# Kernel tuning notes

Hardware: AMD Instinct MI355X
Metric: run time of the kernel (lower is better)

The kernel has to match this reference:

```python
import jax, jax.numpy as jnp
import numpy as np

N_NODES = 50000
N_EDGES = 800000
D = 128
H = 8
HD = D // H
N_NTYPES = 3
N_ETYPES = 5
LN_EPS = 1e-5


def setup_inputs() -> dict:
    key = jax.random.key(0)
    ks = jax.random.split(key, 16)
    inp = {
        "x": jax.random.normal(ks[0], (N_NODES, D), dtype=jnp.float32),
        "edge_index": jax.random.randint(ks[1], (2, N_EDGES), 0, N_NODES),
        "edge_type": jax.random.randint(ks[2], (N_EDGES,), 0, N_ETYPES),
        "node_type": jax.random.randint(ks[3], (N_NODES,), 0, N_NTYPES),
        # per-(node_type, head) QKV projections, per-(edge_type, head) K transform
        "W_Q": jax.random.normal(ks[4], (N_NTYPES, H, HD, HD), dtype=jnp.float32) * 0.02,
        "W_K": jax.random.normal(ks[5], (N_NTYPES, H, HD, HD), dtype=jnp.float32) * 0.02,
        "W_V": jax.random.normal(ks[6], (N_NTYPES, H, HD, HD), dtype=jnp.float32) * 0.02,
        "W_edge": jax.random.normal(ks[7], (N_ETYPES, H, HD, HD), dtype=jnp.float32) * 0.02,
        "mu": jnp.ones((H, N_ETYPES), dtype=jnp.float32),
        "W_out": jax.random.normal(ks[8], (D, D), dtype=jnp.float32) * 0.02,
        "b_out": jnp.zeros((D,), dtype=jnp.float32),
        "ln1_g": jnp.ones((D,), dtype=jnp.float32),
        "ln1_b": jnp.zeros((D,), dtype=jnp.float32),
        "W1": jax.random.normal(ks[9], (D, 4 * D), dtype=jnp.float32) * 0.02,
        "b1": jnp.zeros((4 * D,), dtype=jnp.float32),
        "W2": jax.random.normal(ks[10], (4 * D, D), dtype=jnp.float32) * 0.02,
        "b2": jnp.zeros((D,), dtype=jnp.float32),
        "ln2_g": jnp.ones((D,), dtype=jnp.float32),
        "ln2_b": jnp.zeros((D,), dtype=jnp.float32),
    }
    return inp


def _layer_norm(y, g, b):
    m = y.mean(-1, keepdims=True)
    v = ((y - m) ** 2).mean(-1, keepdims=True)
    return (y - m) * jax.lax.rsqrt(v + LN_EPS) * g + b


def reference(x, edge_index, edge_type, node_type,
              W_Q, W_K, W_V, W_edge, mu,
              W_out, b_out, ln1_g, ln1_b, W1, b1, W2, b2, ln2_g, ln2_b):
    N = x.shape[0]
    xh = x.reshape(N, H, HD)  # heads vectorized (concat of per-head slices)

    # type-specific QKV: small fixed loop over node types, masked select
    Q = jnp.zeros_like(xh)
    K = jnp.zeros_like(xh)
    V = jnp.zeros_like(xh)
    for t in range(N_NTYPES):
        m = (node_type == t)[:, None, None]
        Q = jnp.where(m, jnp.einsum('nhd,hdf->nhf', xh, W_Q[t]), Q)
        K = jnp.where(m, jnp.einsum('nhd,hdf->nhf', xh, W_K[t]), K)
        V = jnp.where(m, jnp.einsum('nhd,hdf->nhf', xh, W_V[t]), V)

    src, dst = edge_index[0], edge_index[1]
    q_dst = Q[dst]   # [E,H,HD]
    k_src = K[src]   # [E,H,HD]

    # edge-type-specific K transform
    kt = jnp.zeros_like(k_src)
    for et in range(N_ETYPES):
        m = (edge_type == et)[:, None, None]
        kt = jnp.where(m, jnp.einsum('ehd,hdf->ehf', k_src, W_edge[et]), kt)

    scores = (q_dst * kt).sum(-1) / jnp.sqrt(jnp.float32(HD))  # [E,H]
    scores = scores * mu[:, edge_type].T                       # mu per edge type, per head

    # sparse softmax over incoming edges of each dst node, per head
    smax = jax.ops.segment_max(scores, dst, num_segments=N)
    ex = jnp.exp(scores - smax[dst])
    den = jax.ops.segment_sum(ex, dst, num_segments=N)
    w = ex / (den[dst] + 1e-10)                                 # [E,H]

    agg = jax.ops.segment_sum(V[src] * w[..., None], dst, num_segments=N)  # [N,H,HD]
    mh = agg.reshape(N, D) @ W_out + b_out  # dropout is identity in eval

    h = _layer_norm(x + mh, ln1_g, ln1_b)
    ffn = jax.nn.gelu(h @ W1 + b1, approximate=False) @ W2 + b2
    return _layer_norm(h + ffn, ln2_g, ln2_b)
```

## Files before the change

### kernel.cpp

```cpp
#include <hip/hip_runtime.h>
#include <hip/hip_bf16.h>

#define N_NODESC 50000
#define N_EDGESC 800000
#define DD 128
#define HH 8
#define HDIM 16
#define N_NT 3
#define N_ET 5
#define NPB 196
#define NEB 400
#define NFB 512
#define WPB 912

#define KV8_OFF    ((size_t)0)
#define QT8_OFF    ((size_t)12800000)
#define XP_OFF     ((size_t)44800000)
#define AGG_OFF    ((size_t)57600000)
#define WOUTT_OFF  ((size_t)83200000)
#define W1T_OFF    ((size_t)83232768)
#define W2T_OFF    ((size_t)83363840)
#define WHPF_OFF   ((size_t)83494912)
#define EDATA_OFF  ((size_t)84183040)
#define ROWS_OFF   ((size_t)87383040)
#define ORIG_OFF   ((size_t)87583104)
#define DEG_OFF    ((size_t)87783104)
#define TOFS_OFF   ((size_t)87983104)
#define BH_OFF     ((size_t)87983168)
#define BB_OFF     ((size_t)87985536)
#define TMP_OFF    ((size_t)87988928)
#define RLOC_OFF   ((size_t)91188928)
#define CSUM_OFF   ((size_t)91389056)

using short8 = __attribute__((ext_vector_type(8))) short;
using f32x4  = __attribute__((ext_vector_type(4))) float;
using f32x2  = __attribute__((ext_vector_type(2))) float;

__device__ __forceinline__ ushort f2b(float f) {
    __hip_bfloat16 h = __float2bfloat16(f);
    return *(ushort*)&h;
}
__device__ __forceinline__ float b2f(ushort u) {
    __hip_bfloat16 h = *(__hip_bfloat16*)&u;
    return __bfloat162float(h);
}
__device__ __forceinline__ f32x2 pk0(unsigned int w) {
    return __builtin_amdgcn_cvt_pk_f32_fp8((int)w, false);
}
__device__ __forceinline__ f32x2 pk1(unsigned int w) {
    return __builtin_amdgcn_cvt_pk_f32_fp8((int)w, true);
}
__device__ __forceinline__ float gelu_f(float v) {
    const float x = v * 0.70710678118654752f;
    const float ax = fabsf(x);
    const float d = fmaf(0.3275911f, ax, 1.0f);
    float t;
    asm("v_rcp_f32 %0, %1" : "=v"(t) : "v"(d));
    float p = fmaf(1.061405429f, t, -1.453152027f);
    p = fmaf(p, t, 1.421413741f);
    p = fmaf(p, t, -0.284496736f);
    p = fmaf(p, t, 0.254829592f);
    p = p * t;
    const float e = __expf(-ax * ax);
    const float er = 1.0f - p * e;
    const float erfx = (x < 0.f) ? -er : er;
    return 0.5f * v * (1.0f + erfx);
}
__device__ __forceinline__ void ebar() {
    __builtin_amdgcn_sched_barrier(0);
    asm volatile("s_waitcnt lgkmcnt(0)" ::: "memory");
    __builtin_amdgcn_sched_barrier(0);
    __builtin_amdgcn_s_barrier();
    __builtin_amdgcn_sched_barrier(0);
}

__global__ __launch_bounds__(256) void prep_a(
    const float* __restrict__ Wout, const float* __restrict__ W1, const float* __restrict__ W2,
    const float* __restrict__ WQ, const float* __restrict__ Wk, const float* __restrict__ Wv,
    const float* __restrict__ We, const float* __restrict__ mu,
    ushort* __restrict__ Woutt, ushort* __restrict__ W1t, ushort* __restrict__ W2t,
    ushort* __restrict__ Whpf,
    const int* __restrict__ ntype, int* __restrict__ bh,
    const int* __restrict__ dst, int* __restrict__ deg, unsigned int* __restrict__ tmp)
{
    const int b = blockIdx.x, tid = threadIdx.x;
    if (b < WPB) {
        const int gid = b * 256 + tid;
        if (gid < 16384) {
            const int nn = gid >> 7, k = gid & 127;
            Woutt[gid] = f2b(Wout[k * 128 + nn]);
        } else if (gid < 81920) {
            const int i = gid - 16384;
            const int nn = i >> 7, k = i & 127;
            W1t[i] = f2b(W1[k * 512 + nn]);
        } else if (gid < 147456) {
            const int i = gid - 81920;
            const int nn = i >> 9, k = i & 511;
            W2t[i] = f2b(W2[k * 128 + nn]);
        } else {
            const int idx = gid - 147456;
            const int t = idx / 28672;
            const int r = idx % 28672;
            const int i = r & 7;
            const int l = (r >> 3) & 63;
            const int f = r >> 9;
            const int j = f % 14, p = f / 14;
            const int c = j * 16 + (l & 15);
            const int k = ((l >> 4) << 3) + i;
            const int hi = (c >= 112) ? 1 : 0;
            const int h = 2 * p + hi;
            float v = 0.f;
            if ((k >> 4) == hi) {
                const int kp = k & 15;
                const int cl = c - hi * 112;
                if (cl < 16) {
                    v = 4.f * Wk[((t * HH + h) * HDIM + kp) * HDIM + cl];
                } else if (cl < 32) {
                    v = 4.f * Wv[((t * HH + h) * HDIM + kp) * HDIM + (cl - 16)];
                } else {
                    const int et = (cl - 32) >> 4, jj = (cl - 32) & 15;
                    const float* wq = WQ + ((t * HH + h) * HDIM + kp) * HDIM;
                    const float* we = We + ((et * HH + h) * HDIM + jj) * HDIM;
                    float s = 0.f;
#pragma unroll
                    for (int ff = 0; ff < 16; ff++) s = fmaf(wq[ff], we[ff], s);
                    v = 64.f * mu[h * N_ET + et] * s;
                }
            }
            Whpf[idx] = f2b(v);
        }
    } else if (b < WPB + NPB) {
        const int bc = b - WPB;
        const int wave = tid >> 6, lane = tid & 63;
        const int n = bc * 256 + tid;
        const int t = (n < N_NODESC) ? ntype[n] : -1;
        const unsigned long long m0 = __ballot(t == 0);
        const unsigned long long m1 = __ballot(t == 1);
        const unsigned long long m2 = __ballot(t == 2);
        __shared__ int wcnt[4][3];
        if (lane == 0) {
            wcnt[wave][0] = (int)__popcll(m0);
            wcnt[wave][1] = (int)__popcll(m1);
            wcnt[wave][2] = (int)__popcll(m2);
        }
        __syncthreads();
        if (tid < 3)
            bh[tid * NPB + bc] = wcnt[0][tid] + wcnt[1][tid] + wcnt[2][tid] + wcnt[3][tid];
    } else {
        for (int e = (b - WPB - NPB) * 256 + tid; e < N_EDGESC; e += NEB * 256) {
            const int nd = dst[e];
            const unsigned int p = (unsigned int)atomicAdd(&deg[nd], 1);
            tmp[e] = (p << 16) | (unsigned int)nd;
        }
    }
}

__global__ __launch_bounds__(256) void prep_b(
    const int* __restrict__ bh, const int* __restrict__ deg,
    int* __restrict__ bb, int* __restrict__ tofs,
    int* __restrict__ rloc, int* __restrict__ csum)
{
    __shared__ int part[256];
    const int tid = threadIdx.x;
    if (blockIdx.x == 0) {
        const int base3 = tid * 3;
        int e0 = (base3 + 0 < 588) ? bh[base3 + 0] : 0;
        int e1 = (base3 + 1 < 588) ? bh[base3 + 1] : 0;
        int e2 = (base3 + 2 < 588) ? bh[base3 + 2] : 0;
        const int l0 = e0, l1 = e0 + e1, l2 = l1 + e2;
        part[tid] = l2;
        __syncthreads();
        for (int off = 1; off < 256; off <<= 1) {
            const int u = (tid >= off) ? part[tid - off] : 0;
            __syncthreads();
            part[tid] += u;
            __syncthreads();
        }
        const int tb = part[tid] - l2;
        if (base3 + 0 < 588) bb[base3 + 0] = tb;
        if (base3 + 1 < 588) bb[base3 + 1] = tb + l0;
        if (base3 + 2 < 588) bb[base3 + 2] = tb + l1;
        __syncthreads();
        if (tid == 0) {
            tofs[0] = 0;
            tofs[1] = bb[NPB];
            tofs[2] = bb[2 * NPB];
            tofs[3] = N_NODESC;
        }
    } else {
        const int c = blockIdx.x - 1;
        const int n = c * 256 + tid;
        const int vdeg = (n < N_NODESC) ? deg[n] : 0;
        part[tid] = vdeg;
        __syncthreads();
        for (int off = 1; off < 256; off <<= 1) {
            const int u = (tid >= off) ? part[tid - off] : 0;
            __syncthreads();
            part[tid] += u;
            __syncthreads();
        }
        if (n <= N_NODESC) rloc[n] = part[tid] - vdeg;
        if (tid == 255) csum[c] = part[255];
    }
}

__global__ __launch_bounds__(256) void prep_c(
    const int* __restrict__ ntype, const float* __restrict__ x,
    const int* __restrict__ src, const int* __restrict__ etype,
    const int* __restrict__ bb, const int* __restrict__ rloc, const int* __restrict__ csum,
    const unsigned int* __restrict__ tmp,
    int* __restrict__ origof, ushort* __restrict__ Xp, int* __restrict__ rows,
    int* __restrict__ edata)
{
    const int b = blockIdx.x, tid = threadIdx.x;
    __shared__ int cb[256];
    {
        const int v = (tid < NPB) ? csum[tid] : 0;
        cb[tid] = v;
        __syncthreads();
        for (int off = 1; off < 256; off <<= 1) {
            const int u = (tid >= off) ? cb[tid - off] : 0;
            __syncthreads();
            cb[tid] += u;
            __syncthreads();
        }
        const int incl = cb[tid];
        __syncthreads();
        cb[tid] = incl - v;
        __syncthreads();
    }

    if (b < NPB) {
        const int wave = tid >> 6, lane = tid & 63;
        const int n = b * 256 + tid;
        const int t = (n < N_NODESC) ? ntype[n] : -1;
        const unsigned long long m0 = __ballot(t == 0);
        const unsigned long long m1 = __ballot(t == 1);
        const unsigned long long m2 = __ballot(t == 2);
        __shared__ int wcnt[4][3];
        __shared__ int sp[256];
        if (lane == 0) {
            wcnt[wave][0] = (int)__popcll(m0);
            wcnt[wave][1] = (int)__popcll(m1);
            wcnt[wave][2] = (int)__popcll(m2);
        }
        __syncthreads();
        int p = -1;
        if (n < N_NODESC) {
            int basew = 0;
#pragma unroll
            for (int w = 0; w < 4; w++) if (w < wave) basew += wcnt[w][t];
            const unsigned long long mt = (t == 0) ? m0 : (t == 1) ? m1 : m2;
            const unsigned long long mlt = ((unsigned long long)1 << lane) - 1;
            p = bb[t * NPB + b] + basew + (int)__popcll(mt & mlt);
            origof[p] = n;
        }
        if (n <= N_NODESC) rows[n] = cb[b] + rloc[n];
        sp[tid] = p;
        __syncthreads();
        for (int i = tid; i < 256 * 16; i += 256) {
            const int nn = i >> 4, c = (i & 15) << 3;
            const int pp = sp[nn];
            if (pp < 0) continue;
            const int n2 = b * 256 + nn;
            const float4 v0 = *(const float4*)(x + (size_t)n2 * DD + c);
            const float4 v1 = *(const float4*)(x + (size_t)n2 * DD + c + 4);
            ushort o[8] = {f2b(v0.x), f2b(v0.y), f2b(v0.z), f2b(v0.w),
                           f2b(v1.x), f2b(v1.y), f2b(v1.z), f2b(v1.w)};
            *(uint4*)(Xp + (size_t)pp * DD + c) = *(uint4*)o;
        }
    } else {
        for (int e = (b - NPB) * 256 + tid; e < N_EDGESC; e += NFB * 256) {
            const unsigned int v = tmp[e];
            const int nd = (int)(v & 0xffffu);
            const int p = (int)(v >> 16);
            edata[cb[nd >> 8] + rloc[nd] + p] = src[e] | (etype[e] << 16);
        }
    }
}

#define LDX 132

__global__ __launch_bounds__(256) void proj_gemm(
    const ushort* __restrict__ Xp, const ushort* __restrict__ Whpf,
    const int* __restrict__ tofs, const int* __restrict__ origof,
    unsigned char* __restrict__ KV8b, unsigned char* __restrict__ Qt8)
{
    const int t = blockIdx.y;
    const int rs = tofs[t], re = tofs[t + 1];
    const int mBase = rs + blockIdx.x * 64;
    if (mBase >= re) return;

    __shared__ ushort Xs[64 * LDX];
    __shared__ ushort Ws[28672];

    const int tid = threadIdx.x;
    const int lane = tid & 63, wave = tid >> 6;
    const int l15 = lane & 15, rq = (lane >> 4) * 4;

#pragma unroll
    for (int it = 0; it < 4; it++) {
        const int idx = it * 256 + tid;
        const int row = idx >> 4, ch = idx & 15;
        int gr = mBase + row; if (gr >= N_NODESC) gr = N_NODESC - 1;
        *(uint4*)&Xs[row * LDX + ch * 8] = *(const uint4*)(Xp + (size_t)gr * DD + ch * 8);
    }
    const ushort* Wg = Whpf + (size_t)t * 28672;
#pragma unroll
    for (int it = 0; it < 14; it++) {
        const int idx = it * 256 + tid;
        *(uint4*)&Ws[idx * 8] = *(const uint4*)(Wg + (size_t)idx * 8);
    }
    __syncthreads();

    int ogr[4]; bool vr[4];
#pragma unroll
    for (int r = 0; r < 4; r++) {
        const int gm = mBase + wave * 16 + rq + r;
        vr[r] = (gm < re);
        ogr[r] = vr[r] ? origof[gm] : 0;
    }

    for (int p = 0; p < 4; p++) {
        const short8 af = *(const short8*)&Xs[(wave * 16 + l15) * LDX + p * 32 + (lane >> 4) * 8];
#pragma unroll
        for (int j = 0; j < 14; j++) {
            const short8 bf = *(const short8*)&Ws[((p * 14 + j) * 64 + lane) * 8];
            f32x4 c = __builtin_amdgcn_mfma_f32_16x16x32_bf16(
                af, bf, (f32x4){0.f, 0.f, 0.f, 0.f}, 0, 0, 0);
            const int hi = (j >= 7) ? 1 : 0;
            const int h = 2 * p + hi;
            const int jj = j - hi * 7;
#pragma unroll
            for (int r = 0; r < 4; r++) {
                if (!vr[r]) continue;
                const float v = c[r];
                const unsigned char b8 =
                    (unsigned char)(__builtin_amdgcn_cvt_pk_fp8_f32(v, v, 0, false) & 0xff);
                const size_t og = (size_t)ogr[r];
                if (jj == 0)      KV8b[og * 256 + h * 16 + l15] = b8;
                else if (jj == 1) KV8b[og * 256 + 128 + h * 16 + l15] = b8;
                else              Qt8[og * 640 + (jj - 2) * 128 + h * 16 + l15] = b8;
            }
        }
    }
}

__global__ __launch_bounds__(128) void edgeagg_kernel(
    const int* __restrict__ rowstart, const int* __restrict__ edata,
    const unsigned char* __restrict__ Qt8, const unsigned char* __restrict__ KV8,
    ushort* __restrict__ agg)
{
    const int w = threadIdx.x >> 6;
    const int lane = threadIdx.x & 63;
    const int n = blockIdx.x * 2 + w;
    const int slot = lane >> 3;
    const int h = lane & 7;

    __shared__ uint4 qs8s[2][40];
    if (lane < 40)
        qs8s[w][lane] = ((const uint4*)(Qt8 + (size_t)n * 640))[lane];
    __syncthreads();
    const uint* qbase = (const uint*)&qs8s[w][0];

    const int s0 = rowstart[n], s1 = rowstart[n + 1];
    const float qsc = 1.44269504f / 1024.f;

    float acc[16];
#pragma unroll
    for (int j = 0; j < 16; j++) acc[j] = 0.f;
    float den = 0.f;

    for (int i = s0 + slot; i < s1; i += 8) {
        const int ed = edata[i];
        const int sn = ed & 0xffff;
        const int et = ed >> 16;
        const unsigned char* kvp = KV8 + ((size_t)sn << 8);
        const uint4 kw = *(const uint4*)(kvp + (h << 4));
        const uint4 vw = *(const uint4*)(kvp + 128 + (h << 4));
        const uint4 qw = *(const uint4*)(qbase + (et << 5) + (h << 2));

        const f32x2 q0 = pk0(qw.x), q1 = pk1(qw.x), q2 = pk0(qw.y), q3 = pk1(qw.y);
        const f32x2 q4 = pk0(qw.z), q5 = pk1(qw.z), q6 = pk0(qw.w), q7 = pk1(qw.w);
        const f32x2 k0 = pk0(kw.x), k1 = pk1(kw.x), k2 = pk0(kw.y), k3 = pk1(kw.y);
        const f32x2 k4 = pk0(kw.z), k5 = pk1(kw.z), k6 = pk0(kw.w), k7 = pk1(kw.w);

        float pa = q0.x * k0.x;
        float pb = q0.y * k0.y;
        float pc = q1.x * k1.x;
        float pd = q1.y * k1.y;
        pa = fmaf(q2.x, k2.x, pa); pb = fmaf(q2.y, k2.y, pb);
        pc = fmaf(q3.x, k3.x, pc); pd = fmaf(q3.y, k3.y, pd);
        pa = fmaf(q4.x, k4.x, pa); pb = fmaf(q4.y, k4.y, pb);
        pc = fmaf(q5.x, k5.x, pc); pd = fmaf(q5.y, k5.y, pd);
        pa = fmaf(q6.x, k6.x, pa); pb = fmaf(q6.y, k6.y, pb);
        pc = fmaf(q7.x, k7.x, pc); pd = fmaf(q7.y, k7.y, pd);

        const float ex = exp2f(((pa + pb) + (pc + pd)) * qsc);
        den += ex;

        const f32x2 v0 = pk0(vw.x), v1 = pk1(vw.x), v2 = pk0(vw.y), v3 = pk1(vw.y);
        const f32x2 v4 = pk0(vw.z), v5 = pk1(vw.z), v6 = pk0(vw.w), v7 = pk1(vw.w);
        acc[0]  = fmaf(ex, v0.x, acc[0]);  acc[1]  = fmaf(ex, v0.y, acc[1]);
        acc[2]  = fmaf(ex, v1.x, acc[2]);  acc[3]  = fmaf(ex, v1.y, acc[3]);
        acc[4]  = fmaf(ex, v2.x, acc[4]);  acc[5]  = fmaf(ex, v2.y, acc[5]);
        acc[6]  = fmaf(ex, v3.x, acc[6]);  acc[7]  = fmaf(ex, v3.y, acc[7]);
        acc[8]  = fmaf(ex, v4.x, acc[8]);  acc[9]  = fmaf(ex, v4.y, acc[9]);
        acc[10] = fmaf(ex, v5.x, acc[10]); acc[11] = fmaf(ex, v5.y, acc[11]);
        acc[12] = fmaf(ex, v6.x, acc[12]); acc[13] = fmaf(ex, v6.y, acc[13]);
        acc[14] = fmaf(ex, v7.x, acc[14]); acc[15] = fmaf(ex, v7.y, acc[15]);
    }

    {
        const int b0 = slot & 1, b1 = slot & 2, b2 = slot & 4;
#pragma unroll
        for (int j = 0; j < 8; j++) {
            const float v = b0 ? acc[j] : acc[j + 8];
            const float r = __shfl_xor(v, 8);
            acc[j] = (b0 ? acc[j + 8] : acc[j]) + r;
        }
#pragma unroll
        for (int j = 0; j < 4; j++) {
            const float v = b1 ? acc[j] : acc[j + 4];
            const float r = __shfl_xor(v, 16);
            acc[j] = (b1 ? acc[j + 4] : acc[j]) + r;
        }
#pragma unroll
        for (int j = 0; j < 2; j++) {
            const float v = b2 ? acc[j] : acc[j + 2];
            const float r = __shfl_xor(v, 32);
            acc[j] = (b2 ? acc[j + 2] : acc[j]) + r;
        }
        den += __shfl_xor(den, 8);
        den += __shfl_xor(den, 16);
        den += __shfl_xor(den, 32);
    }
    const float rr = 0.25f / (den + 1e-10f);
    const int fb = (h << 4) + ((slot & 1) << 3) + ((slot & 2) << 1) + ((slot & 4) >> 1);
    ushort o2[2] = { f2b(acc[0] * rr), f2b(acc[1] * rr) };
    *(uint*)&agg[((size_t)n << 7) + fb] = *(uint*)o2;
}

#define LDH 132
#define LDB2 68

#define LOADB(P0, P1, PTR) { P0 = *(const short8*)(PTR); P1 = *(const short8*)((PTR) + 8); }
#define STAGEB(BUF, P0, P1) { *(short8*)&Bs[BUF][br * LDB2 + bc] = P0; \
                              *(short8*)&Bs[BUF][br * LDB2 + bc + 8] = P1; }

__global__ __launch_bounds__(512, 4) void fused_tail(
    const ushort* __restrict__ agg, const ushort* __restrict__ Woutt,
    const ushort* __restrict__ W1t, const ushort* __restrict__ W2t,
    const float* __restrict__ x,
    const float* __restrict__ bout, const float* __restrict__ g1, const float* __restrict__ b1ln,
    const float* __restrict__ b1, const float* __restrict__ b2,
    const float* __restrict__ g2, const float* __restrict__ b2ln,
    float* __restrict__ out)
{
    __shared__ ushort Bs[2][128 * LDB2];
    __shared__ ushort Hs[64 * LDH];
    __shared__ ushort Ts[64 * LDH];
    __shared__ float red[2][4][64];

    const int tid = threadIdx.x;
    const int lane = tid & 63, wave = tid >> 6;
    const int wm = wave >> 2, wn = wave & 3;
    const int l15 = lane & 15, q8 = (lane >> 4) * 8, rq = (lane >> 4) * 4;
    const int mBase = blockIdx.x * 64;

    const int br = tid >> 2, bc = (tid & 3) * 16;
    const int ar = tid >> 3, ac = (tid & 7) * 16;
    int rowA = mBase + ar; if (rowA >= N_NODESC) rowA = N_NODESC - 1;

    f32x4 acc1[2][2], acc2[2][2];
#pragma unroll
    for (int i = 0; i < 2; i++)
#pragma unroll
        for (int j = 0; j < 2; j++) {
            acc1[i][j] = (f32x4){0.f, 0.f, 0.f, 0.f};
            acc2[i][j] = (f32x4){0.f, 0.f, 0.f, 0.f};
        }

    short8 pX0, pX1, pY0, pY1, aT0, aT1;
    LOADB(pX0, pX1, Woutt + (size_t)br * 128 + bc);
    LOADB(pY0, pY1, Woutt + (size_t)br * 128 + 64 + bc);
    aT0 = *(const short8*)(agg + (size_t)rowA * DD + ac);
    aT1 = *(const short8*)(agg + (size_t)rowA * DD + ac + 8);
    float xv[2][4][2];
#pragma unroll
    for (int i = 0; i < 2; i++)
#pragma unroll
        for (int r = 0; r < 4; r++) {
            const int gm = mBase + wm * 32 + i * 16 + rq + r;
            const int gr = (gm < N_NODESC) ? gm : N_NODESC - 1;
#pragma unroll
            for (int j = 0; j < 2; j++)
                xv[i][r][j] = x[(size_t)gr * DD + wn * 32 + j * 16 + l15];
        }
    *(short8*)&Ts[ar * LDH + ac] = aT0;
    *(short8*)&Ts[ar * LDH + ac + 8] = aT1;
    STAGEB(0, pX0, pX1);
    LOADB(pX0, pX1, W1t + (size_t)br * 128 + bc);
    ebar();

    STAGEB(1, pY0, pY1);
    LOADB(pY0, pY1, W1t + (size_t)br * 128 + 64 + bc);
#pragma unroll
    for (int kk2 = 0; kk2 < 2; kk2++) {
        short8 af[2], bf[2];
#pragma unroll
        for (int i = 0; i < 2; i++)
            af[i] = *(const short8*)&Ts[(wm * 32 + i * 16 + l15) * LDH + kk2 * 32 + q8];
#pragma unroll
        for (int j = 0; j < 2; j++)
            bf[j] = *(const short8*)&Bs[0][(wn * 32 + j * 16 + l15) * LDB2 + kk2 * 32 + q8];
#pragma unroll
        for (int i = 0; i < 2; i++)
#pragma unroll
            for (int j = 0; j < 2; j++)
                acc1[i][j] = __builtin_amdgcn_mfma_f32_16x16x32_bf16(af[i], bf[j], acc1[i][j], 0, 0, 0);
    }
    ebar();

    STAGEB(0, pX0, pX1);
    LOADB(pX0, pX1, W2t + (size_t)br * 512 + bc);
#pragma unroll
    for (int kk2 = 0; kk2 < 2; kk2++) {
        short8 af[2], bf[2];
#pragma unroll
        for (int i = 0; i < 2; i++)
            af[i] = *(const short8*)&Ts[(wm * 32 + i * 16 + l15) * LDH + 64 + kk2 * 32 + q8];
#pragma unroll
        for (int j = 0; j < 2; j++)
            bf[j] = *(const short8*)&Bs[1][(wn * 32 + j * 16 + l15) * LDB2 + kk2 * 32 + q8];
#pragma unroll
        for (int i = 0; i < 2; i++)
#pragma unroll
            for (int j = 0; j < 2; j++)
                acc1[i][j] = __builtin_amdgcn_mfma_f32_16x16x32_bf16(af[i], bf[j], acc1[i][j], 0, 0, 0);
    }
    ebar();

    {
        float bo[2], gv[2], bv[2];
#pragma unroll
        for (int j = 0; j < 2; j++) {
            const int gn = wn * 32 + j * 16 + l15;
            bo[j] = bout[gn]; gv[j] = g1[gn]; bv[j] = b1ln[gn];
        }
#pragma unroll
        for (int i = 0; i < 2; i++) {
#pragma unroll
            for (int r = 0; r < 4; r++) {
                const int row = wm * 32 + i * 16 + rq + r;
                float s = 0.f, ss = 0.f;
#pragma unroll
                for (int j = 0; j < 2; j++) {
                    float v = acc1[i][j][r] + bo[j] + xv[i][r][j];
                    acc1[i][j][r] = v;
                    s += v; ss += v * v;
                }
                s  += __shfl_xor(s, 1);  s  += __shfl_xor(s, 2);  s  += __shfl_xor(s, 4);  s  += __shfl_xor(s, 8);
                ss += __shfl_xor(ss, 1); ss += __shfl_xor(ss, 2); ss += __shfl_xor(ss, 4); ss += __shfl_xor(ss, 8);
                if (l15 == 0) { red[0][wn][row] = s; red[1][wn][row] = ss; }
            }
        }
        ebar();
#pragma unroll
        for (int i = 0; i < 2; i++) {
#pragma unroll
            for (int r = 0; r < 4; r++) {
                const int row = wm * 32 + i * 16 + rq + r;
                const float s  = red[0][0][row] + red[0][1][row] + red[0][2][row] + red[0][3][row];
                const float ss = red[1][0][row] + red[1][1][row] + red[1][2][row] + red[1][3][row];
                const float mean = s * (1.f / 128.f);
                const float var  = ss * (1.f / 128.f) - mean * mean;
                const float rstd = rsqrtf(var + 1e-5f);
#pragma unroll
                for (int j = 0; j < 2; j++) {
                    const int gn = wn * 32 + j * 16 + l15;
                    Hs[row * LDH + gn] = f2b((acc1[i][j][r] - mean) * rstd * gv[j] + bv[j]);
                }
            }
        }
        ebar();
    }

    for (int nb = 0; nb < 4; nb++) {
        f32x4 a1[2][2];
#pragma unroll
        for (int i = 0; i < 2; i++)
#pragma unroll
            for (int j = 0; j < 2; j++) a1[i][j] = (f32x4){0.f, 0.f, 0.f, 0.f};

        STAGEB(1, pY0, pY1);
        LOADB(pY0, pY1, W2t + (size_t)br * 512 + nb * 128 + 64 + bc);
#pragma unroll
        for (int kk2 = 0; kk2 < 2; kk2++) {
            short8 af[2], bf[2];
#pragma unroll
            for (int i = 0; i < 2; i++)
                af[i] = *(const short8*)&Hs[(wm * 32 + i * 16 + l15) * LDH + kk2 * 32 + q8];
#pragma unroll
            for (int j = 0; j < 2; j++)
                bf[j] = *(const short8*)&Bs[0][(wn * 32 + j * 16 + l15) * LDB2 + kk2 * 32 + q8];
#pragma unroll
            for (int i = 0; i < 2; i++)
#pragma unroll
                for (int j = 0; j < 2; j++)
                    a1[i][j] = __builtin_amdgcn_mfma_f32_16x16x32_bf16(af[i], bf[j], a1[i][j], 0, 0, 0);
        }
        ebar();

        STAGEB(0, pX0, pX1);
        if (nb < 3) { LOADB(pX0, pX1, W1t + (size_t)((nb + 1) * 128 + br) * 128 + bc); }
#pragma unroll
        for (int kk2 = 0; kk2 < 2; kk2++) {
            short8 af[2], bf[2];
#pragma unroll
            for (int i = 0; i < 2; i++)
                af[i] = *(const short8*)&Hs[(wm * 32 + i * 16 + l15) * LDH + 64 + kk2 * 32 + q8];
#pragma unroll
            for (int j = 0; j < 2; j++)
                bf[j] = *(const short8*)&Bs[1][(wn * 32 + j * 16 + l15) * LDB2 + kk2 * 32 + q8];
#pragma unroll
            for (int i = 0; i < 2; i++)
#pragma unroll
                for (int j = 0; j < 2; j++)
                    a1[i][j] = __builtin_amdgcn_mfma_f32_16x16x32_bf16(af[i], bf[j], a1[i][j], 0, 0, 0);
        }
        ebar();

        {
            float b1v[2];
#pragma unroll
            for (int j = 0; j < 2; j++)
                b1v[j] = b1[nb * 128 + wn * 32 + j * 16 + l15];
#pragma unroll
            for (int i = 0; i < 2; i++)
#pragma unroll
                for (int j = 0; j < 2; j++)
#pragma unroll
                    for (int r = 0; r < 4; r++) {
                        const int row = wm * 32 + i * 16 + rq + r;
                        const int col = wn * 32 + j * 16 + l15;
                        Ts[row * LDH + col] = f2b(gelu_f(a1[i][j][r] + b1v[j]));
                    }
        }
        ebar();

        STAGEB(1, pY0, pY1);
        if (nb < 3) { LOADB(pY0, pY1, W1t + (size_t)((nb + 1) * 128 + br) * 128 + 64 + bc); }
#pragma unroll
        for (int kk2 = 0; kk2 < 2; kk2++) {
            short8 af[2], bf[2];
#pragma unroll
            for (int i = 0; i < 2; i++)
                af[i] = *(const short8*)&Ts[(wm * 32 + i * 16 + l15) * LDH + kk2 * 32 + q8];
#pragma unroll
            for (int j = 0; j < 2; j++)
                bf[j] = *(const short8*)&Bs[0][(wn * 32 + j * 16 + l15) * LDB2 + kk2 * 32 + q8];
#pragma unroll
            for (int i = 0; i < 2; i++)
#pragma unroll
                for (int j = 0; j < 2; j++)
                    acc2[i][j] = __builtin_amdgcn_mfma_f32_16x16x32_bf16(af[i], bf[j], acc2[i][j], 0, 0, 0);
        }
        ebar();

        if (nb < 3) {
            STAGEB(0, pX0, pX1);
            LOADB(pX0, pX1, W2t + (size_t)br * 512 + (nb + 1) * 128 + bc);
        }
#pragma unroll
        for (int kk2 = 0; kk2 < 2; kk2++) {
            short8 af[2], bf[2];
#pragma unroll
            for (int i = 0; i < 2; i++)
                af[i] = *(const short8*)&Ts[(wm * 32 + i * 16 + l15) * LDH + 64 + kk2 * 32 + q8];
#pragma unroll
            for (int j = 0; j < 2; j++)
                bf[j] = *(const short8*)&Bs[1][(wn * 32 + j * 16 + l15) * LDB2 + kk2 * 32 + q8];
#pragma unroll
            for (int i = 0; i < 2; i++)
#pragma unroll
                for (int j = 0; j < 2; j++)
                    acc2[i][j] = __builtin_amdgcn_mfma_f32_16x16x32_bf16(af[i], bf[j], acc2[i][j], 0, 0, 0);
        }
        ebar();
    }

    {
        float b2v[2], gv[2], bv[2];
#pragma unroll
        for (int j = 0; j < 2; j++) {
            const int gn = wn * 32 + j * 16 + l15;
            b2v[j] = b2[gn]; gv[j] = g2[gn]; bv[j] = b2ln[gn];
        }
#pragma unroll
        for (int i = 0; i < 2; i++) {
#pragma unroll
            for (int r = 0; r < 4; r++) {
                const int row = wm * 32 + i * 16 + rq + r;
                float s = 0.f, ss = 0.f;
#pragma unroll
                for (int j = 0; j < 2; j++) {
                    const int gn = wn * 32 + j * 16 + l15;
                    float v = acc2[i][j][r] + b2v[j] + b2f(Hs[row * LDH + gn]);
                    acc2[i][j][r] = v;
                    s += v; ss += v * v;
                }
                s  += __shfl_xor(s, 1);  s  += __shfl_xor(s, 2);  s  += __shfl_xor(s, 4);  s  += __shfl_xor(s, 8);
                ss += __shfl_xor(ss, 1); ss += __shfl_xor(ss, 2); ss += __shfl_xor(ss, 4); ss += __shfl_xor(ss, 8);
                if (l15 == 0) { red[0][wn][row] = s; red[1][wn][row] = ss; }
            }
        }
        ebar();
#pragma unroll
        for (int i = 0; i < 2; i++) {
#pragma unroll
            for (int r = 0; r < 4; r++) {
                const int row = wm * 32 + i * 16 + rq + r;
                const int gm = mBase + row;
                if (gm >= N_NODESC) continue;
                const float s  = red[0][0][row] + red[0][1][row] + red[0][2][row] + red[0][3][row];
                const float ss = red[1][0][row] + red[1][1][row] + red[1][2][row] + red[1][3][row];
                const float mean = s * (1.f / 128.f);
                const float var  = ss * (1.f / 128.f) - mean * mean;
                const float rstd = rsqrtf(var + 1e-5f);
#pragma unroll
                for (int j = 0; j < 2; j++) {
                    const int gn = wn * 32 + j * 16 + l15;
                    out[(size_t)gm * DD + gn] = (acc2[i][j][r] - mean) * rstd * gv[j] + bv[j];
                }
            }
        }
    }
}

extern "C" void kernel_launch(void* const* d_in, const int* in_sizes, int n_in,
                              void* d_out, int out_size, void* d_ws, size_t ws_size,
                              hipStream_t stream)
{
    const float* x     = (const float*)d_in[0];
    const int*   ei    = (const int*)d_in[1];
    const int*   etyp  = (const int*)d_in[2];
    const int*   ntype = (const int*)d_in[3];
    const float* Wq    = (const float*)d_in[4];
    const float* Wk    = (const float*)d_in[5];
    const float* Wv    = (const float*)d_in[6];
    const float* We    = (const float*)d_in[7];
    const float* mu    = (const float*)d_in[8];
    const float* Wout  = (const float*)d_in[9];
    const float* bout  = (const float*)d_in[10];
    const float* g1    = (const float*)d_in[11];
    const float* b1ln  = (const float*)d_in[12];
    const float* W1    = (const float*)d_in[13];
    const float* b1    = (const float*)d_in[14];
    const float* W2    = (const float*)d_in[15];
    const float* b2    = (const float*)d_in[16];
    const float* g2    = (const float*)d_in[17];
    const float* b2ln  = (const float*)d_in[18];
    float* out = (float*)d_out;

    char* ws = (char*)d_ws;
    ushort*        KV8   = (ushort*)(ws + KV8_OFF);
    unsigned char* Qt8   = (unsigned char*)(ws + QT8_OFF);
    ushort*        Xp    = (ushort*)(ws + XP_OFF);
    ushort*        agg   = (ushort*)(ws + AGG_OFF);
    ushort*        Woutt = (ushort*)(ws + WOUTT_OFF);
    ushort*        W1t   = (ushort*)(ws + W1T_OFF);
    ushort*        W2t   = (ushort*)(ws + W2T_OFF);
    ushort*        Whpf  = (ushort*)(ws + WHPF_OFF);
    int*           edata = (int*)(ws + EDATA_OFF);
    int*           rows  = (int*)(ws + ROWS_OFF);
    int*           origof= (int*)(ws + ORIG_OFF);
    int*           deg   = (int*)(ws + DEG_OFF);
    int*           tofs  = (int*)(ws + TOFS_OFF);
    int*           bh    = (int*)(ws + BH_OFF);
    int*           bb    = (int*)(ws + BB_OFF);
    unsigned int*  tmp   = (unsigned int*)(ws + TMP_OFF);
    int*           rloc  = (int*)(ws + RLOC_OFF);
    int*           csum  = (int*)(ws + CSUM_OFF);

    const int* srcA = ei;
    const int* dstA = ei + N_EDGESC;

    (void)hipMemsetAsync(ws + DEG_OFF, 0, 200000, stream);

    prep_a<<<WPB + NPB + NEB, 256, 0, stream>>>(
        Wout, W1, W2, Wq, Wk, Wv, We, mu, Woutt, W1t, W2t, Whpf,
        ntype, bh, dstA, deg, tmp);
    prep_b<<<1 + NPB, 256, 0, stream>>>(bh, deg, bb, tofs, rloc, csum);
    prep_c<<<NPB + NFB, 256, 0, stream>>>(ntype, x, srcA, etyp, bb, rloc, csum, tmp,
                                          origof, Xp, rows, edata);

    proj_gemm<<<dim3(782, 3), 256, 0, stream>>>(Xp, Whpf, tofs, origof,
                                                (unsigned char*)KV8, Qt8);
    edgeagg_kernel<<<N_NODESC / 2, 128, 0, stream>>>(rows, edata, Qt8,
                                                     (const unsigned char*)KV8, agg);

    fused_tail<<<782, 512, 0, stream>>>(agg, Woutt, W1t, W2t, x,
                                        bout, g1, b1ln, b1, b2, g2, b2ln, out);
}
```

Baseline: 310.3 us.

## Gather x directly in projection GEMM and prefetch next edge in aggregation

```diff
diff --git a/kernel.cpp b/kernel.cpp
--- a/kernel.cpp
+++ b/kernel.cpp
@@ -15,7 +15,6 @@
 
 #define KV8_OFF    ((size_t)0)
 #define QT8_OFF    ((size_t)12800000)
-#define XP_OFF     ((size_t)44800000)
 #define AGG_OFF    ((size_t)57600000)
 #define WOUTT_OFF  ((size_t)83200000)
 #define W1T_OFF    ((size_t)83232768)
@@ -205,11 +204,11 @@
 }
 
 __global__ __launch_bounds__(256) void prep_c(
-    const int* __restrict__ ntype, const float* __restrict__ x,
+    const int* __restrict__ ntype,
     const int* __restrict__ src, const int* __restrict__ etype,
     const int* __restrict__ bb, const int* __restrict__ rloc, const int* __restrict__ csum,
     const unsigned int* __restrict__ tmp,
-    int* __restrict__ origof, ushort* __restrict__ Xp, int* __restrict__ rows,
+    int* __restrict__ origof, int* __restrict__ rows,
     int* __restrict__ edata)
 {
     const int b = blockIdx.x, tid = threadIdx.x;
@@ -238,37 +237,22 @@
         const unsigned long long m1 = __ballot(t == 1);
         const unsigned long long m2 = __ballot(t == 2);
         __shared__ int wcnt[4][3];
-        __shared__ int sp[256];
         if (lane == 0) {
             wcnt[wave][0] = (int)__popcll(m0);
             wcnt[wave][1] = (int)__popcll(m1);
             wcnt[wave][2] = (int)__popcll(m2);
         }
         __syncthreads();
-        int p = -1;
         if (n < N_NODESC) {
             int basew = 0;
 #pragma unroll
             for (int w = 0; w < 4; w++) if (w < wave) basew += wcnt[w][t];
             const unsigned long long mt = (t == 0) ? m0 : (t == 1) ? m1 : m2;
             const unsigned long long mlt = ((unsigned long long)1 << lane) - 1;
-            p = bb[t * NPB + b] + basew + (int)__popcll(mt & mlt);
+            const int p = bb[t * NPB + b] + basew + (int)__popcll(mt & mlt);
             origof[p] = n;
         }
         if (n <= N_NODESC) rows[n] = cb[b] + rloc[n];
-        sp[tid] = p;
-        __syncthreads();
-        for (int i = tid; i < 256 * 16; i += 256) {
-            const int nn = i >> 4, c = (i & 15) << 3;
-            const int pp = sp[nn];
-            if (pp < 0) continue;
-            const int n2 = b * 256 + nn;
-            const float4 v0 = *(const float4*)(x + (size_t)n2 * DD + c);
-            const float4 v1 = *(const float4*)(x + (size_t)n2 * DD + c + 4);
-            ushort o[8] = {f2b(v0.x), f2b(v0.y), f2b(v0.z), f2b(v0.w),
-                           f2b(v1.x), f2b(v1.y), f2b(v1.z), f2b(v1.w)};
-            *(uint4*)(Xp + (size_t)pp * DD + c) = *(uint4*)o;
-        }
     } else {
         for (int e = (b - NPB) * 256 + tid; e < N_EDGESC; e += NFB * 256) {
             const unsigned int v = tmp[e];
@@ -282,7 +266,7 @@
 #define LDX 132
 
 __global__ __launch_bounds__(256) void proj_gemm(
-    const ushort* __restrict__ Xp, const ushort* __restrict__ Whpf,
+    const float* __restrict__ x, const ushort* __restrict__ Whpf,
     const int* __restrict__ tofs, const int* __restrict__ origof,
     unsigned char* __restrict__ KV8b, unsigned char* __restrict__ Qt8)
 {
@@ -302,8 +286,13 @@
     for (int it = 0; it < 4; it++) {
         const int idx = it * 256 + tid;
         const int row = idx >> 4, ch = idx & 15;
-        int gr = mBase + row; if (gr >= N_NODESC) gr = N_NODESC - 1;
-        *(uint4*)&Xs[row * LDX + ch * 8] = *(const uint4*)(Xp + (size_t)gr * DD + ch * 8);
+        int gm = mBase + row; if (gm >= N_NODESC) gm = N_NODESC - 1;
+        const int og = origof[gm];
+        const float4 v0 = *(const float4*)(x + (size_t)og * DD + ch * 8);
+        const float4 v1 = *(const float4*)(x + (size_t)og * DD + ch * 8 + 4);
+        ushort o[8] = {f2b(v0.x), f2b(v0.y), f2b(v0.z), f2b(v0.w),
+                       f2b(v1.x), f2b(v1.y), f2b(v1.z), f2b(v1.w)};
+        *(uint4*)&Xs[row * LDX + ch * 8] = *(uint4*)o;
     }
     const ushort* Wg = Whpf + (size_t)t * 28672;
 #pragma unroll
@@ -371,13 +360,27 @@
     for (int j = 0; j < 16; j++) acc[j] = 0.f;
     float den = 0.f;
 
-    for (int i = s0 + slot; i < s1; i += 8) {
-        const int ed = edata[i];
-        const int sn = ed & 0xffff;
+    int i = s0 + slot;
+    int ed = 0;
+    uint4 kw = {0u, 0u, 0u, 0u}, vw = {0u, 0u, 0u, 0u};
+    if (i < s1) {
+        ed = edata[i];
+        const unsigned char* kvp = KV8 + ((size_t)(ed & 0xffff) << 8);
+        kw = *(const uint4*)(kvp + (h << 4));
+        vw = *(const uint4*)(kvp + 128 + (h << 4));
+    }
+    while (i < s1) {
+        const int in2 = i + 8;
+        int edn = 0;
+        uint4 kwn = {0u, 0u, 0u, 0u}, vwn = {0u, 0u, 0u, 0u};
+        if (in2 < s1) {
+            edn = edata[in2];
+            const unsigned char* kvpn = KV8 + ((size_t)(edn & 0xffff) << 8);
+            kwn = *(const uint4*)(kvpn + (h << 4));
+            vwn = *(const uint4*)(kvpn + 128 + (h << 4));
+        }
+
         const int et = ed >> 16;
-        const unsigned char* kvp = KV8 + ((size_t)sn << 8);
-        const uint4 kw = *(const uint4*)(kvp + (h << 4));
-        const uint4 vw = *(const uint4*)(kvp + 128 + (h << 4));
         const uint4 qw = *(const uint4*)(qbase + (et << 5) + (h << 2));
 
         const f32x2 q0 = pk0(qw.x), q1 = pk1(qw.x), q2 = pk0(qw.y), q3 = pk1(qw.y);
@@ -409,6 +412,8 @@
         acc[10] = fmaf(ex, v5.x, acc[10]); acc[11] = fmaf(ex, v5.y, acc[11]);
         acc[12] = fmaf(ex, v6.x, acc[12]); acc[13] = fmaf(ex, v6.y, acc[13]);
         acc[14] = fmaf(ex, v7.x, acc[14]); acc[15] = fmaf(ex, v7.y, acc[15]);
+
+        i = in2; ed = edn; kw = kwn; vw = vwn;
     }
 
     {
@@ -766,7 +771,6 @@
     char* ws = (char*)d_ws;
     ushort*        KV8   = (ushort*)(ws + KV8_OFF);
     unsigned char* Qt8   = (unsigned char*)(ws + QT8_OFF);
-    ushort*        Xp    = (ushort*)(ws + XP_OFF);
     ushort*        agg   = (ushort*)(ws + AGG_OFF);
     ushort*        Woutt = (ushort*)(ws + WOUTT_OFF);
     ushort*        W1t   = (ushort*)(ws + W1T_OFF);
@@ -792,10 +796,10 @@
         Wout, W1, W2, Wq, Wk, Wv, We, mu, Woutt, W1t, W2t, Whpf,
         ntype, bh, dstA, deg, tmp);
     prep_b<<<1 + NPB, 256, 0, stream>>>(bh, deg, bb, tofs, rloc, csum);
-    prep_c<<<NPB + NFB, 256, 0, stream>>>(ntype, x, srcA, etyp, bb, rloc, csum, tmp,
-                                          origof, Xp, rows, edata);
-
-    proj_gemm<<<dim3(782, 3), 256, 0, stream>>>(Xp, Whpf, tofs, origof,
+    prep_c<<<NPB + NFB, 256, 0, stream>>>(ntype, srcA, etyp, bb, rloc, csum, tmp,
+                                          origof, rows, edata);
+
+    proj_gemm<<<dim3(782, 3), 256, 0, stream>>>(x, Whpf, tofs, origof,
                                                 (unsigned char*)KV8, Qt8);
     edgeagg_kernel<<<N_NODESC / 2, 128, 0, stream>>>(rows, edata, Qt8,
                                                      (const unsigned char*)KV8, agg);
```

Measured after the change: 309.3 us. No clear change (-0.3%).
